# Kernel optimization log

Measured on AMD Instinct MI355X. Metric: run time of the kernel, lower is better.

The kernel has to match this reference:

```python
import jax, jax.numpy as jnp
import numpy as np

TEMPERATURE = 0.5


def setup_inputs() -> dict:
    key = jax.random.key(0)
    k1, k2 = jax.random.split(key)
    N, D = 4096, 512
    emb_i = jax.random.normal(k1, (N, D), dtype=jnp.float32)
    emb_j = jax.random.normal(k2, (N, D), dtype=jnp.float32)
    return {"emb_i": emb_i, "emb_j": emb_j}


def reference(emb_i, emb_j):
    # L2-normalize each embedding row (F.normalize, dim=1)
    z_i = emb_i / jnp.linalg.norm(emb_i, axis=1, keepdims=True)
    z_j = emb_j / jnp.linalg.norm(emb_j, axis=1, keepdims=True)
    reps = jnp.concatenate([z_i, z_j], axis=0)  # [2N, D]
    N = emb_i.shape[0]
    M = 2 * N
    # cosine similarity of normalized vectors == dot product -> [2N, 2N]
    sim = jnp.einsum('id,jd->ij', reps, reps) / TEMPERATURE
    # denominator: sum_k!=i exp(sim[i,k]); original multiplies by one-hot complement
    exp_sim = jnp.exp(sim)
    denom = jnp.sum(exp_sim, axis=1) - jnp.diagonal(exp_sim)  # [2N]
    log_denom = jnp.log(denom)
    # positive pairs: (k, k+N) and (k+N, k)
    idx = jnp.arange(N)
    pos_ij = sim[idx, idx + N]          # sim(k, k+N)/T
    pos_ji = sim[idx + N, idx]          # sim(k+N, k)/T
    loss = jnp.sum(-(pos_ij - log_denom[:N]) - (pos_ji - log_denom[N:]))
    return loss / (2.0 * N)
```

## Files before the change

### kernel.cpp

```cpp
#include <hip/hip_runtime.h>
#include <cstdint>
#include <cstddef>

constexpr int N_ROWS = 4096;
constexpr int D      = 512;
constexpr int M      = 8192;
constexpr int NTILE  = 64;
constexpr int NBLK   = NTILE * (NTILE + 1) / 2;
constexpr int NKT    = 8;

using f32x16 = __attribute__((ext_vector_type(16))) float;
using i32x4  = __attribute__((ext_vector_type(4))) int;
using i32x8  = __attribute__((ext_vector_type(8))) int;

#define SS_FP8(pk, accum)                                                           \
    do {                                                                            \
        float f0 = __builtin_amdgcn_cvt_f32_fp8((pk), 0);                           \
        float f1 = __builtin_amdgcn_cvt_f32_fp8((pk), 1);                           \
        float f2 = __builtin_amdgcn_cvt_f32_fp8((pk), 2);                           \
        float f3 = __builtin_amdgcn_cvt_f32_fp8((pk), 3);                           \
        (accum) += f0 * f0 + f1 * f1 + f2 * f2 + f3 * f3;                           \
    } while (0)


__global__ __launch_bounds__(256) void normpos_kernel(
    const float* __restrict__ emb_i, const float* __restrict__ emb_j,
    uint8_t* __restrict__ zb, float* __restrict__ diagss,
    float* __restrict__ pos)
{
    const int wave = threadIdx.x >> 6, lane = threadIdx.x & 63;
    const int k = blockIdx.x * 4 + wave;

    const float4* a = (const float4*)(emb_i + (size_t)k * D);
    const float4* b = (const float4*)(emb_j + (size_t)k * D);
    float4 a0 = a[lane * 2], a1 = a[lane * 2 + 1];
    float4 b0 = b[lane * 2], b1 = b[lane * 2 + 1];

    float ssi = a0.x*a0.x + a0.y*a0.y + a0.z*a0.z + a0.w*a0.w
              + a1.x*a1.x + a1.y*a1.y + a1.z*a1.z + a1.w*a1.w;
    float ssj = b0.x*b0.x + b0.y*b0.y + b0.z*b0.z + b0.w*b0.w
              + b1.x*b1.x + b1.y*b1.y + b1.z*b1.z + b1.w*b1.w;
    float dp  = a0.x*b0.x + a0.y*b0.y + a0.z*b0.z + a0.w*b0.w
              + a1.x*b1.x + a1.y*b1.y + a1.z*b1.z + a1.w*b1.w;
    #pragma unroll
    for (int off = 32; off; off >>= 1) {
        ssi += __shfl_xor(ssi, off, 64);
        ssj += __shfl_xor(ssj, off, 64);
        dp  += __shfl_xor(dp,  off, 64);
    }
    const float invi = rsqrtf(ssi), invj = rsqrtf(ssj);

    const float zi[8] = {a0.x*invi, a0.y*invi, a0.z*invi, a0.w*invi,
                         a1.x*invi, a1.y*invi, a1.z*invi, a1.w*invi};
    const float zj[8] = {b0.x*invj, b0.y*invj, b0.z*invj, b0.w*invj,
                         b1.x*invj, b1.y*invj, b1.z*invj, b1.w*invj};

    int pi0 = __builtin_amdgcn_cvt_pk_fp8_f32(zi[0], zi[1], 0, false);
    pi0     = __builtin_amdgcn_cvt_pk_fp8_f32(zi[2], zi[3], pi0, true);
    int pi1 = __builtin_amdgcn_cvt_pk_fp8_f32(zi[4], zi[5], 0, false);
    pi1     = __builtin_amdgcn_cvt_pk_fp8_f32(zi[6], zi[7], pi1, true);
    int pj0 = __builtin_amdgcn_cvt_pk_fp8_f32(zj[0], zj[1], 0, false);
    pj0     = __builtin_amdgcn_cvt_pk_fp8_f32(zj[2], zj[3], pj0, true);
    int pj1 = __builtin_amdgcn_cvt_pk_fp8_f32(zj[4], zj[5], 0, false);
    pj1     = __builtin_amdgcn_cvt_pk_fp8_f32(zj[6], zj[7], pj1, true);

    float dssi = 0.f, dssj = 0.f;
    SS_FP8(pi0, dssi);
    SS_FP8(pi1, dssi);
    SS_FP8(pj0, dssj);
    SS_FP8(pj1, dssj);

    const size_t off8 = (size_t)((k >> 5) * 8 + (lane >> 3)) * 2048
                      + (size_t)(((lane >> 1) & 1)) * 1024
                      + (size_t)(((k & 31) * 2 + ((lane >> 2) & 1))) * 16
                      + (size_t)((lane & 1)) * 8;
    const unsigned long long vi =
        ((unsigned long long)(unsigned)pi1 << 32) | (unsigned)pi0;
    const unsigned long long vj =
        ((unsigned long long)(unsigned)pj1 << 32) | (unsigned)pj0;
    *(unsigned long long*)(zb + off8)                       = vi;
    *(unsigned long long*)(zb + off8 + (size_t)N_ROWS * D)  = vj;

    #pragma unroll
    for (int off = 32; off; off >>= 1) {
        dssi += __shfl_xor(dssi, off, 64);
        dssj += __shfl_xor(dssj, off, 64);
    }
    if (lane == 0) {
        diagss[k]          = dssi;
        diagss[k + N_ROWS] = dssj;
        pos[k]             = 2.0f * dp * invi * invj;
    }
}

__global__ __launch_bounds__(256, 3) void simgemm_kernel(
    const uint8_t* __restrict__ zb, float* __restrict__ partials)
{
    __shared__ float rp[4][64];
    __shared__ float cp4[4][64];

    const int tid  = threadIdx.x;
    const int wave = tid >> 6, lane = tid & 63;
    const int l31  = lane & 31, half = lane >> 5;

    const int t = blockIdx.x;
    int bi = (int)((129.0f - sqrtf(129.0f * 129.0f - 8.0f * (float)t)) * 0.5f);
    while (bi > 0 && bi * (129 - bi) / 2 > t) --bi;
    while ((bi + 1) * (129 - (bi + 1)) / 2 <= t) ++bi;
    const int bj = bi + (t - bi * (129 - bi) / 2);
    const bool diag = (bi == bj);

    const int wr = wave >> 1, wc = wave & 1;

    const int lofs = ((l31 << 1) | half) * 16;
    const uint8_t* baseA0 = zb + (size_t)(bi * 4 + wr * 2    ) * 8 * 2048 + lofs;
    const uint8_t* baseA1 = zb + (size_t)(bi * 4 + wr * 2 + 1) * 8 * 2048 + lofs;
    const uint8_t* baseB0 = zb + (size_t)(bj * 4 + wc * 2    ) * 8 * 2048 + lofs;
    const uint8_t* baseB1 = zb + (size_t)(bj * 4 + wc * 2 + 1) * 8 * 2048 + lofs;

#define LDFRAG(DST, BP, IT)                                                         \
    do {                                                                            \
        i32x4 _lo = *(const i32x4*)((BP) + (size_t)(IT) * 2048);                    \
        i32x4 _hi = *(const i32x4*)((BP) + (size_t)(IT) * 2048 + 1024);             \
        DST = __builtin_shufflevector(_lo, _hi, 0, 1, 2, 3, 4, 5, 6, 7);            \
    } while (0)

    f32x16 acc[2][2] = {};
    i32x8 fA0[2], fA1[2], fB0[2], fB1[2];

    LDFRAG(fA0[0], baseA0, 0);
    LDFRAG(fA1[0], baseA1, 0);
    LDFRAG(fB0[0], baseB0, 0);
    LDFRAG(fB1[0], baseB1, 0);

    #pragma unroll
    for (int it = 0; it < NKT; ++it) {
        const int cur = it & 1, nxt = cur ^ 1;
        if (it + 1 < NKT) {
            LDFRAG(fA0[nxt], baseA0, it + 1);
            LDFRAG(fA1[nxt], baseA1, it + 1);
            LDFRAG(fB0[nxt], baseB0, it + 1);
            LDFRAG(fB1[nxt], baseB1, it + 1);
        }
        acc[0][0] = __builtin_amdgcn_mfma_scale_f32_32x32x64_f8f6f4(
            fA0[cur], fB0[cur], acc[0][0], 0, 0, 0, 0x7f7f7f7f, 0, 0x7f7f7f7f);
        acc[0][1] = __builtin_amdgcn_mfma_scale_f32_32x32x64_f8f6f4(
            fA0[cur], fB1[cur], acc[0][1], 0, 0, 0, 0x7f7f7f7f, 0, 0x7f7f7f7f);
        acc[1][0] = __builtin_amdgcn_mfma_scale_f32_32x32x64_f8f6f4(
            fA1[cur], fB0[cur], acc[1][0], 0, 0, 0, 0x7f7f7f7f, 0, 0x7f7f7f7f);
        acc[1][1] = __builtin_amdgcn_mfma_scale_f32_32x32x64_f8f6f4(
            fA1[cur], fB1[cur], acc[1][1], 0, 0, 0, 0x7f7f7f7f, 0, 0x7f7f7f7f);
    }

    float rowp[2][16] = {};
    #pragma unroll
    for (int j = 0; j < 2; ++j) {
        float cpj = 0.f;
        #pragma unroll
        for (int i = 0; i < 2; ++i)
            #pragma unroll
            for (int r = 0; r < 16; ++r) {
                float e = __expf(2.0f * acc[i][j][r]);
                rowp[i][r] += e;
                cpj += e;
            }
        if (!diag) {
            cpj += __shfl_xor(cpj, 32, 64);
            if (half == 0) cp4[wave][j * 32 + l31] = cpj;
        }
    }
    #pragma unroll
    for (int i = 0; i < 2; ++i)
        #pragma unroll
        for (int r = 0; r < 16; ++r) {
            float e = rowp[i][r];
            e += __shfl_xor(e, 1, 64);
            e += __shfl_xor(e, 2, 64);
            e += __shfl_xor(e, 4, 64);
            e += __shfl_xor(e, 8, 64);
            e += __shfl_xor(e, 16, 64);
            if (l31 == 0)
                rp[wave][i * 32 + (r & 3) + 8 * (r >> 2) + 4 * half] = e;
        }
    __syncthreads();

    float* pA = partials + (size_t)(bi * NTILE + bj) * 128;
    float* pB = partials + (size_t)(bj * NTILE + bi) * 128;
    if (tid < 128) {
        const int h = tid >> 6, rr = tid & 63;
        pA[tid] = rp[h * 2][rr] + rp[h * 2 + 1][rr];
    } else if (!diag) {
        const int c = tid - 128, h = c >> 6, cc = c & 63;
        pB[c] = cp4[h][cc] + cp4[h + 2][cc];
    }
}

__global__ __launch_bounds__(256) void rowfin_kernel(
    const float* __restrict__ partials, const float* __restrict__ diagss,
    const float* __restrict__ pos, float* __restrict__ lgpart)
{
    const int r  = blockIdx.x;
    const int ri = threadIdx.x & 127;
    const int ch = threadIdx.x >> 7;
    const float* base = partials + (size_t)r * NTILE * 128 + ri;
    float s = 0.f;
    #pragma unroll
    for (int c = 0; c < 32; ++c)
        s += base[(size_t)(ch * 32 + c) * 128];
    __shared__ float half1[128];
    __shared__ float red[4];
    if (ch == 1) half1[ri] = s;
    __syncthreads();
    float lg = 0.f;
    if (ch == 0) {
        float rs = s + half1[ri];
        int row = r * 128 + ri;
        lg = __logf(rs - __expf(2.0f * diagss[row]));
    }
    if (threadIdx.x < 64)
        lg -= 2.0f * pos[r * 64 + threadIdx.x];
    #pragma unroll
    for (int off = 32; off; off >>= 1) lg += __shfl_xor(lg, off, 64);
    const int wave = threadIdx.x >> 6, lane = threadIdx.x & 63;
    if (lane == 0) red[wave] = lg;
    __syncthreads();
    if (threadIdx.x == 0) lgpart[r] = red[0] + red[1] + red[2] + red[3];
}

__global__ __launch_bounds__(64) void loss_kernel(
    const float* __restrict__ lgpart, float* __restrict__ out)
{
    float local = lgpart[threadIdx.x];
    #pragma unroll
    for (int off = 32; off; off >>= 1) local += __shfl_xor(local, off, 64);
    if (threadIdx.x == 0) out[0] = local * (1.0f / 8192.0f);
}

extern "C" void kernel_launch(void* const* d_in, const int* in_sizes, int n_in,
                              void* d_out, int out_size, void* d_ws, size_t ws_size,
                              hipStream_t stream)
{
    const float* emb_i = (const float*)d_in[0];
    const float* emb_j = (const float*)d_in[1];

    uint8_t* zb = (uint8_t*)d_ws;
    float* partials = (float*)((char*)d_ws + (size_t)M * D);
    float* diagss   = partials + (size_t)NTILE * NTILE * 128;
    float* pos      = diagss + M;
    float* lgpart   = pos + N_ROWS;
    float* out      = (float*)d_out;

    normpos_kernel<<<N_ROWS / 4, 256, 0, stream>>>(emb_i, emb_j, zb, diagss, pos);
    simgemm_kernel<<<NBLK, 256, 0, stream>>>(zb, partials);
    rowfin_kernel<<<NTILE, 256, 0, stream>>>(partials, diagss, pos, lgpart);
    loss_kernel<<<1, 64, 0, stream>>>(lgpart, out);
}
```

Measured before the change: 108.5 us.

## Remap block order, relax occupancy, and explicitly pipeline MFMA fragment loads

The GEMM kernel's k-loop now uses two named fragment buffers in a ping-pong pattern. Scheduling barriers force the next loads to be issued before each group of four MFMAs, so memory latency overlaps with compute. The triangular tile index is remapped so consecutive block IDs are spread across eight strided segments, which changes L2/XCD locality. Launch bounds drop from 3 to 2 blocks per CU, giving the compiler more registers at the risk of lower occupancy.

```diff
diff --git a/kernel.cpp b/kernel.cpp
--- a/kernel.cpp
+++ b/kernel.cpp
@@ -93,7 +93,7 @@
     }
 }
 
-__global__ __launch_bounds__(256, 3) void simgemm_kernel(
+__global__ __launch_bounds__(256, 2) void simgemm_kernel(
     const uint8_t* __restrict__ zb, float* __restrict__ partials)
 {
     __shared__ float rp[4][64];
@@ -103,7 +103,7 @@
     const int wave = tid >> 6, lane = tid & 63;
     const int l31  = lane & 31, half = lane >> 5;
 
-    const int t = blockIdx.x;
+    const int t = ((int)(blockIdx.x & 7)) * (NBLK / 8) + ((int)blockIdx.x >> 3);
     int bi = (int)((129.0f - sqrtf(129.0f * 129.0f - 8.0f * (float)t)) * 0.5f);
     while (bi > 0 && bi * (129 - bi) / 2 > t) --bi;
     while ((bi + 1) * (129 - (bi + 1)) / 2 <= t) ++bi;
@@ -125,31 +125,46 @@
         DST = __builtin_shufflevector(_lo, _hi, 0, 1, 2, 3, 4, 5, 6, 7);            \
     } while (0)
 
+#define MFMA4(A0, A1, B0, B1)                                                       \
+    do {                                                                            \
+        acc[0][0] = __builtin_amdgcn_mfma_scale_f32_32x32x64_f8f6f4(                \
+            A0, B0, acc[0][0], 0, 0, 0, 0x7f7f7f7f, 0, 0x7f7f7f7f);                 \
+        acc[0][1] = __builtin_amdgcn_mfma_scale_f32_32x32x64_f8f6f4(                \
+            A0, B1, acc[0][1], 0, 0, 0, 0x7f7f7f7f, 0, 0x7f7f7f7f);                 \
+        acc[1][0] = __builtin_amdgcn_mfma_scale_f32_32x32x64_f8f6f4(                \
+            A1, B0, acc[1][0], 0, 0, 0, 0x7f7f7f7f, 0, 0x7f7f7f7f);                 \
+        acc[1][1] = __builtin_amdgcn_mfma_scale_f32_32x32x64_f8f6f4(                \
+            A1, B1, acc[1][1], 0, 0, 0, 0x7f7f7f7f, 0, 0x7f7f7f7f);                 \
+    } while (0)
+
     f32x16 acc[2][2] = {};
-    i32x8 fA0[2], fA1[2], fB0[2], fB1[2];
-
-    LDFRAG(fA0[0], baseA0, 0);
-    LDFRAG(fA1[0], baseA1, 0);
-    LDFRAG(fB0[0], baseB0, 0);
-    LDFRAG(fB1[0], baseB1, 0);
-
-    #pragma unroll
-    for (int it = 0; it < NKT; ++it) {
-        const int cur = it & 1, nxt = cur ^ 1;
+    i32x8 cA0, cA1, cB0, cB1;
+    i32x8 nA0, nA1, nB0, nB1;
+
+    LDFRAG(cA0, baseA0, 0);
+    LDFRAG(cA1, baseA1, 0);
+    LDFRAG(cB0, baseB0, 0);
+    LDFRAG(cB1, baseB1, 0);
+
+    #pragma unroll
+    for (int it = 0; it < NKT; it += 2) {
         if (it + 1 < NKT) {
-            LDFRAG(fA0[nxt], baseA0, it + 1);
-            LDFRAG(fA1[nxt], baseA1, it + 1);
-            LDFRAG(fB0[nxt], baseB0, it + 1);
-            LDFRAG(fB1[nxt], baseB1, it + 1);
-        }
-        acc[0][0] = __builtin_amdgcn_mfma_scale_f32_32x32x64_f8f6f4(
-            fA0[cur], fB0[cur], acc[0][0], 0, 0, 0, 0x7f7f7f7f, 0, 0x7f7f7f7f);
-        acc[0][1] = __builtin_amdgcn_mfma_scale_f32_32x32x64_f8f6f4(
-            fA0[cur], fB1[cur], acc[0][1], 0, 0, 0, 0x7f7f7f7f, 0, 0x7f7f7f7f);
-        acc[1][0] = __builtin_amdgcn_mfma_scale_f32_32x32x64_f8f6f4(
-            fA1[cur], fB0[cur], acc[1][0], 0, 0, 0, 0x7f7f7f7f, 0, 0x7f7f7f7f);
-        acc[1][1] = __builtin_amdgcn_mfma_scale_f32_32x32x64_f8f6f4(
-            fA1[cur], fB1[cur], acc[1][1], 0, 0, 0, 0x7f7f7f7f, 0, 0x7f7f7f7f);
+            LDFRAG(nA0, baseA0, it + 1);
+            LDFRAG(nA1, baseA1, it + 1);
+            LDFRAG(nB0, baseB0, it + 1);
+            LDFRAG(nB1, baseB1, it + 1);
+        }
+        __builtin_amdgcn_sched_barrier(0);
+        MFMA4(cA0, cA1, cB0, cB1);
+
+        if (it + 2 < NKT) {
+            LDFRAG(cA0, baseA0, it + 2);
+            LDFRAG(cA1, baseA1, it + 2);
+            LDFRAG(cB0, baseB0, it + 2);
+            LDFRAG(cB1, baseB1, it + 2);
+        }
+        __builtin_amdgcn_sched_barrier(0);
+        MFMA4(nA0, nA1, nB0, nB1);
     }
 
     float rowp[2][16] = {};
```

New measurement: 104.6 us. -3.5%, faster.
